# Kernel tuning notes

Hardware: AMD Instinct MI355X
Metric: run time of the kernel (lower is better)

Reference implementation:

```python
import jax, jax.numpy as jnp
import numpy as np

D_MODEL = 2048
HEADS = 16
D_K = D_MODEL // HEADS  # 128
BATCH = 4
SEQ = 2048


def setup_inputs() -> dict:
    key = jax.random.key(0)
    ks = jax.random.split(key, 5)
    scale = (2.0 / (D_MODEL + D_MODEL)) ** 0.5  # trunc-normal std from init
    return {
        "x": jax.random.normal(ks[0], (BATCH, SEQ, D_MODEL), dtype=jnp.float32),
        "W_Q": jax.random.normal(ks[1], (D_MODEL, D_MODEL), dtype=jnp.float32) * scale,
        "W_K": jax.random.normal(ks[2], (D_MODEL, D_MODEL), dtype=jnp.float32) * scale,
        "W_V": jax.random.normal(ks[3], (D_MODEL, D_MODEL), dtype=jnp.float32) * scale,
        "W_O": jax.random.normal(ks[4], (D_MODEL, D_MODEL), dtype=jnp.float32) * scale,
    }


def reference(x, W_Q, W_K, W_V, W_O):
    b, s, d = x.shape
    # weights stored as [(h d_k), d_model] -> [h, d_k, d_model]
    wq = W_Q.reshape(HEADS, D_K, d)
    wk = W_K.reshape(HEADS, D_K, d)
    wv = W_V.reshape(HEADS, D_K, d)
    # projections: [b, h, s, d_k]
    Q = jnp.einsum("hkd,bsd->bhsk", wq, x)
    K = jnp.einsum("hkd,bsd->bhsk", wk, x)
    V = jnp.einsum("hvd,bsd->bhsv", wv, x)
    # causal scaled dot-product attention
    scores = jnp.einsum("bhqk,bhsk->bhqs", Q, K) / jnp.sqrt(jnp.asarray(D_K, x.dtype))
    causal = jnp.tril(jnp.ones((s, s), dtype=bool))  # True -> attend
    scores = jnp.where(causal, scores, jnp.asarray(-jnp.inf, x.dtype))
    attn = jax.nn.softmax(scores, axis=-1)
    mh = jnp.einsum("bhqs,bhsv->bhqv", attn, V)  # [b, h, s, d_v]
    # concat heads -> [b, s, h*d_v]
    mh = jnp.transpose(mh, (0, 2, 1, 3)).reshape(b, s, HEADS * D_K)
    # output projection: W_O is [d_model, (h d_v)]
    out = jnp.einsum("dm,bsm->bsd", W_O, mh)
    return out
```

## Files before the change

### kernel.cpp

```cpp
#include <hip/hip_runtime.h>
#include <stdint.h>

#define D_MODEL 2048
#define HEADS   16
#define DKH     128
#define BATCH   4
#define SEQ     2048
#define MROWS   (BATCH*SEQ)

typedef unsigned short u16;
typedef __attribute__((ext_vector_type(8))) short   short8;
typedef __attribute__((ext_vector_type(4))) float   floatx4;

#define Q_PRESCALE 0.12751744509914576f

__device__ __forceinline__ u16 f2bf(float f) {
  unsigned u = __float_as_uint(f);
  u += 0x7fffu + ((u >> 16) & 1u);
  return (u16)(u >> 16);
}
__device__ __forceinline__ u16 f2bf_fast(float f) {
  return (u16)((__float_as_uint(f) + 0x8000u) >> 16);
}

__device__ __forceinline__ void async_lds16(const u16* g, u16* l) {
  __builtin_amdgcn_global_load_lds(
      (const __attribute__((address_space(1))) unsigned int*)g,
      (__attribute__((address_space(3))) unsigned int*)l, 16, 0, 0);
}

__global__ void cast_all(const float4* __restrict__ x,  const float4* __restrict__ wq,
                         const float4* __restrict__ wk, const float4* __restrict__ wv,
                         const float4* __restrict__ wo, ushort4* __restrict__ dst) {
  int i = blockIdx.x * blockDim.x + threadIdx.x;
  int stride = gridDim.x * blockDim.x;
  for (; i < 8388608; i += stride) {
    const float4* s; int j;
    if (i < 4194304) { s = x; j = i; }
    else {
      int t = i - 4194304; int w = t >> 20; j = t & 1048575;
      s = (w == 0) ? wq : (w == 1) ? wk : (w == 2) ? wv : wo;
    }
    float4 f = s[j];
    ushort4 o;
    o.x = f2bf(f.x); o.y = f2bf(f.y); o.z = f2bf(f.z); o.w = f2bf(f.w);
    dst[i] = o;
  }
}

#define KDIM 2048
#define NKT  32

#define STAGE_A(t, buf) do { \
    const size_t go = (size_t)(t) * 64; \
    const int bo = (buf) * 32768; \
    async_lds16(sA0 + go,          dL0 + bo); \
    async_lds16(sA1 + go,          dL1 + bo); \
    async_lds16(sA0 + go + 262144, dL0 + bo + 8192); \
    async_lds16(sA1 + go + 262144, dL1 + bo + 8192); \
  } while (0)
#define STAGE_B(t, buf) do { \
    const size_t go = (size_t)(t) * 64; \
    const int bo = (buf) * 32768; \
    async_lds16(sB0 + go,          dL0 + bo + 16384); \
    async_lds16(sB1 + go,          dL1 + bo + 16384); \
    async_lds16(sB0 + go + 262144, dL0 + bo + 24576); \
    async_lds16(sB1 + go + 262144, dL1 + bo + 24576); \
  } while (0)

__device__ __forceinline__ void gemm256_core(
    const u16* __restrict__ A, const u16* __restrict__ B,
    u16* __restrict__ S, int rowBase, int colBase, floatx4 acc[8][4])
{
  const int tid  = threadIdx.x;
  const int lane = tid & 63;
  const int w    = tid >> 6;
  const int wm   = w >> 2, wn = w & 3;
  const int c    = lane & 15, quad = lane >> 4;

  const u16 *sA0, *sA1, *sB0, *sB1;
  {
    int L0 = tid * 16, L1 = 8192 + tid * 16;
    int Ls0 = L0 ^ (((L0 >> 7) & 7) << 4);
    int Ls1 = L1 ^ (((L1 >> 7) & 7) << 4);
    sA0 = A + (size_t)(rowBase + (Ls0 >> 7)) * KDIM + ((Ls0 & 127) >> 1);
    sA1 = A + (size_t)(rowBase + (Ls1 >> 7)) * KDIM + ((Ls1 & 127) >> 1);
    sB0 = B + (size_t)(colBase + (Ls0 >> 7)) * KDIM + ((Ls0 & 127) >> 1);
    sB1 = B + (size_t)(colBase + (Ls1 >> 7)) * KDIM + ((Ls1 & 127) >> 1);
  }
  u16* dL0 = S + tid * 8;
  u16* dL1 = S + 4096 + tid * 8;

  const int fo0 = (c * 128 + ((       quad * 16) ^ ((c & 7) << 4))) >> 1;
  const int fo1 = (c * 128 + ((64 +   quad * 16) ^ ((c & 7) << 4))) >> 1;
  const u16* aW = S + wm * 8192;
  const u16* bW = S + 16384 + (wn >> 1) * 8192 + (wn & 1) * 4096;

  const floatx4 z4 = {0.f, 0.f, 0.f, 0.f};
#pragma unroll
  for (int i = 0; i < 8; i++)
#pragma unroll
    for (int j = 0; j < 4; j++) acc[i][j] = z4;

  STAGE_A(0, 0); STAGE_B(0, 0);
  STAGE_A(1, 1); STAGE_B(1, 1);
  asm volatile("s_waitcnt vmcnt(8)" ::: "memory");
  __builtin_amdgcn_s_barrier();

  short8 af[4][2], bf01[2][2], bf23[2][2];

  for (int t = 0; t < NKT; ++t) {
    const int b = t & 1;
    const u16* aB = aW + b * 32768;
    const u16* bB = bW + b * 32768;

#pragma unroll
    for (int i = 0; i < 4; i++) {
      af[i][0] = *(const short8*)(aB + i * 1024 + fo0);
      af[i][1] = *(const short8*)(aB + i * 1024 + fo1);
    }
#pragma unroll
    for (int j = 0; j < 2; j++) {
      bf01[j][0] = *(const short8*)(bB + j * 1024 + fo0);
      bf01[j][1] = *(const short8*)(bB + j * 1024 + fo1);
    }
    if (t >= 1 && t + 1 < NKT) STAGE_B(t + 1, b ^ 1);
    __builtin_amdgcn_s_barrier();
    asm volatile("s_waitcnt lgkmcnt(0)" ::: "memory");
    __builtin_amdgcn_sched_barrier(0);
    __builtin_amdgcn_s_setprio(1);
#pragma unroll
    for (int i = 0; i < 4; i++)
#pragma unroll
      for (int j = 0; j < 2; j++) {
        acc[i][j] = __builtin_amdgcn_mfma_f32_16x16x32_bf16(af[i][0], bf01[j][0], acc[i][j], 0, 0, 0);
        acc[i][j] = __builtin_amdgcn_mfma_f32_16x16x32_bf16(af[i][1], bf01[j][1], acc[i][j], 0, 0, 0);
      }
    __builtin_amdgcn_s_setprio(0);
    __builtin_amdgcn_s_barrier();

#pragma unroll
    for (int j = 0; j < 2; j++) {
      bf23[j][0] = *(const short8*)(bB + (2 + j) * 1024 + fo0);
      bf23[j][1] = *(const short8*)(bB + (2 + j) * 1024 + fo1);
    }
    __builtin_amdgcn_s_barrier();
    asm volatile("s_waitcnt lgkmcnt(0)" ::: "memory");
    __builtin_amdgcn_sched_barrier(0);
    __builtin_amdgcn_s_setprio(1);
#pragma unroll
    for (int i = 0; i < 4; i++)
#pragma unroll
      for (int j = 0; j < 2; j++) {
        acc[i][2 + j] = __builtin_amdgcn_mfma_f32_16x16x32_bf16(af[i][0], bf23[j][0], acc[i][2 + j], 0, 0, 0);
        acc[i][2 + j] = __builtin_amdgcn_mfma_f32_16x16x32_bf16(af[i][1], bf23[j][1], acc[i][2 + j], 0, 0, 0);
      }
    __builtin_amdgcn_s_setprio(0);
    __builtin_amdgcn_s_barrier();

#pragma unroll
    for (int i = 0; i < 4; i++) {
      af[i][0] = *(const short8*)(aB + (4 + i) * 1024 + fo0);
      af[i][1] = *(const short8*)(aB + (4 + i) * 1024 + fo1);
    }
    __builtin_amdgcn_s_barrier();
    asm volatile("s_waitcnt lgkmcnt(0)" ::: "memory");
    __builtin_amdgcn_sched_barrier(0);
    __builtin_amdgcn_s_setprio(1);
#pragma unroll
    for (int i = 0; i < 4; i++)
#pragma unroll
      for (int j = 0; j < 2; j++) {
        acc[4 + i][2 + j] = __builtin_amdgcn_mfma_f32_16x16x32_bf16(af[i][0], bf23[j][0], acc[4 + i][2 + j], 0, 0, 0);
        acc[4 + i][2 + j] = __builtin_amdgcn_mfma_f32_16x16x32_bf16(af[i][1], bf23[j][1], acc[4 + i][2 + j], 0, 0, 0);
      }
    __builtin_amdgcn_s_setprio(0);
    __builtin_amdgcn_s_barrier();

    if (t + 2 < NKT) STAGE_A(t + 2, b);
    __builtin_amdgcn_s_barrier();
    __builtin_amdgcn_s_setprio(1);
#pragma unroll
    for (int i = 0; i < 4; i++)
#pragma unroll
      for (int j = 0; j < 2; j++) {
        acc[4 + i][j] = __builtin_amdgcn_mfma_f32_16x16x32_bf16(af[i][0], bf01[j][0], acc[4 + i][j], 0, 0, 0);
        acc[4 + i][j] = __builtin_amdgcn_mfma_f32_16x16x32_bf16(af[i][1], bf01[j][1], acc[4 + i][j], 0, 0, 0);
      }
    __builtin_amdgcn_s_setprio(0);
    asm volatile("s_waitcnt vmcnt(4)" ::: "memory");
    __builtin_amdgcn_s_barrier();
  }
}

__global__ __launch_bounds__(512, 2) void gemm_qkv(
    const u16* __restrict__ A, const u16* __restrict__ B,
    u16* __restrict__ Qb, u16* __restrict__ Kb, u16* __restrict__ Vpb)
{
  __shared__ __align__(16) u16 S[65536];

  const int tid  = threadIdx.x;
  const int lane = tid & 63;
  const int w    = tid >> 6;
  const int wm   = w >> 2, wn = w & 3;
  const int c    = lane & 15, quad = lane >> 4;
  const int rowBase = blockIdx.x * 256;
  const int colBase = blockIdx.y * 256;

  floatx4 acc[8][4];
  gemm256_core(A, B, S, rowBase, colBase, acc);

  const int proj = colBase >> 11;
  const float esc = (proj == 0) ? Q_PRESCALE : 1.0f;
  u16* dst = (proj == 0) ? Qb : (proj == 1) ? Kb : Vpb;

#pragma unroll
  for (int i = 0; i < 8; i++) {
#pragma unroll
    for (int j = 0; j < 4; j++) {
#pragma unroll
      for (int r = 0; r < 4; r++) {
        int row = rowBase + wm * 128 + i * 16 + quad * 4 + r;
        int col = (colBase & 2047) + wn * 64 + j * 16 + c;
        float v = acc[i][j][r] * esc;
        if (proj < 2) {
          size_t idx = ((size_t)((row >> 11) * HEADS + (col >> 7)) * SEQ + (row & 2047)) * DKH + (col & 127);
          dst[idx] = f2bf(v);
        } else {
          int srow = row & 2047;
          int sp = (srow & ~127) | (((srow & 15) << 3) | ((srow >> 4) & 7));
          size_t idx = ((size_t)((row >> 11) * HEADS + (col >> 7)) * DKH + (col & 127)) * SEQ + sp;
          dst[idx] = f2bf(v);
        }
      }
    }
  }
}

__global__ __launch_bounds__(512, 2) void gemm_out(
    const u16* __restrict__ A, const u16* __restrict__ B,
    float* __restrict__ Cout)
{
  __shared__ __align__(16) u16 S[65536];

  const int tid  = threadIdx.x;
  const int lane = tid & 63;
  const int w    = tid >> 6;
  const int wm   = w >> 2, wn = w & 3;
  const int c    = lane & 15, quad = lane >> 4;
  const int rowBase = blockIdx.x * 256;
  const int colBase = blockIdx.y * 256;

  floatx4 acc[8][4];
  gemm256_core(A, B, S, rowBase, colBase, acc);

#pragma unroll
  for (int i = 0; i < 8; i++)
#pragma unroll
    for (int j = 0; j < 4; j++)
#pragma unroll
      for (int r = 0; r < 4; r++) {
        int row = rowBase + wm * 128 + i * 16 + quad * 4 + r;
        int col = colBase + wn * 64 + j * 16 + c;
        Cout[(size_t)row * D_MODEL + col] = acc[i][j][r];
      }
}

__global__ __launch_bounds__(256, 1) void attn_fwd(
    const u16* __restrict__ Qg, const u16* __restrict__ Kg,
    const u16* __restrict__ Vpg, u16* __restrict__ mh)
{
  __shared__ __align__(16) u16 Sh[2 * 16384 + 16384 + 4 * 32 * 136];

  const int tid  = threadIdx.x;
  const int lane = tid & 63;
  const int w    = tid >> 6;
  const int c    = lane & 15, quad = lane >> 4;
  const int bh   = blockIdx.x;
  const int qt   = 15 - blockIdx.y;
  const int q0   = qt * 128;

  const u16* Qbh = Qg  + (size_t)bh * SEQ * DKH;
  const u16* Kbh = Kg  + (size_t)bh * SEQ * DKH;
  const u16* Vbh = Vpg + (size_t)bh * DKH * SEQ;

  u16* Vs = Sh + 32768;
  u16* Pw = Sh + 49152 + w * 32 * 136;

  const int rowb = tid >> 4;
  const int cbh  = (((tid & 15) ^ (rowb & 7)) << 3);
  const u16* sK = Kbh + rowb * DKH + cbh;
  const u16* sV = Vbh + (size_t)rowb * SEQ + cbh;

  int fof[4];
#pragma unroll
  for (int ks = 0; ks < 4; ks++)
    fof[ks] = ((ks * 64 + quad * 16) ^ ((c & 7) << 4)) >> 1;

#define STAGE_K_ATTN(kbN, buf) do { \
    u16* d_ = Sh + (buf) * 16384 + tid * 8; \
    const u16* s_ = sK + (size_t)(kbN) * DKH; \
    _Pragma("unroll") \
    for (int q_ = 0; q_ < 8; q_++) async_lds16(s_ + q_ * 2048, d_ + q_ * 2048); \
  } while (0)
#define STAGE_V_ATTN(kb_) do { \
    u16* d_ = Vs + tid * 8; \
    const u16* s_ = sV + (kb_); \
    _Pragma("unroll") \
    for (int q_ = 0; q_ < 8; q_++) async_lds16(s_ + (size_t)q_ * 16 * SEQ, d_ + q_ * 2048); \
  } while (0)

  short8 qf[2][4];
#pragma unroll
  for (int m2 = 0; m2 < 2; m2++)
#pragma unroll
    for (int ks = 0; ks < 4; ks++)
      qf[m2][ks] = *(const short8*)&Qbh[(size_t)(q0 + w * 32 + m2 * 16 + c) * DKH + ks * 32 + quad * 8];

  const floatx4 z4 = {0.f, 0.f, 0.f, 0.f};
  floatx4 oacc[2][8];
#pragma unroll
  for (int m2 = 0; m2 < 2; m2++)
#pragma unroll
    for (int d = 0; d < 8; d++) oacc[m2][d] = z4;
  float lrow[2][4];
#pragma unroll
  for (int m2 = 0; m2 < 2; m2++)
#pragma unroll
    for (int r = 0; r < 4; r++) lrow[m2][r] = 0.f;

  STAGE_K_ATTN(0, 0);
  __syncthreads();

  for (int kt = 0; kt <= qt; kt++) {
    const int kb = kt * 128;
    const u16* Kc = Sh + (kt & 1) * 16384;

    STAGE_V_ATTN(kb);
    if (kt < qt) STAGE_K_ATTN(kb + 128, (kt + 1) & 1);

    short8 kf[4][8];
#pragma unroll
    for (int ks = 0; ks < 4; ks++)
#pragma unroll
      for (int n = 0; n < 8; n++)
        kf[ks][n] = *(const short8*)&Kc[(n * 16 + c) * 128 + fof[ks]];

    floatx4 s[2][8];
#pragma unroll
    for (int m2 = 0; m2 < 2; m2++)
#pragma unroll
      for (int n = 0; n < 8; n++) s[m2][n] = z4;
#pragma unroll
    for (int ks = 0; ks < 4; ks++)
#pragma unroll
      for (int n = 0; n < 8; n++) {
        s[0][n] = __builtin_amdgcn_mfma_f32_16x16x32_bf16(qf[0][ks], kf[ks][n], s[0][n], 0, 0, 0);
        s[1][n] = __builtin_amdgcn_mfma_f32_16x16x32_bf16(qf[1][ks], kf[ks][n], s[1][n], 0, 0, 0);
      }

    if (kt == qt) {
#pragma unroll
      for (int m2 = 0; m2 < 2; m2++)
#pragma unroll
        for (int n = 0; n < 8; n++)
#pragma unroll
          for (int r = 0; r < 4; r++) {
            int qrow = w * 32 + m2 * 16 + quad * 4 + r;
            int key  = n * 16 + c;
            if (key > qrow) s[m2][n][r] = -3.0e38f;
          }
    }

#pragma unroll
    for (int m2 = 0; m2 < 2; m2++) {
#pragma unroll
      for (int r = 0; r < 4; r++) {
        float rs = 0.f;
#pragma unroll
        for (int n = 0; n < 8; n++) {
          float p = __builtin_amdgcn_exp2f(s[m2][n][r]);
          s[m2][n][r] = p;
          rs += p;
        }
        rs += __shfl_xor(rs, 1);
        rs += __shfl_xor(rs, 2);
        rs += __shfl_xor(rs, 4);
        rs += __shfl_xor(rs, 8);
        lrow[m2][r] += rs;
      }
    }

#pragma unroll
    for (int m2 = 0; m2 < 2; m2++) {
#pragma unroll
      for (int r = 0; r < 4; r++) {
        short8 pk;
#pragma unroll
        for (int n = 0; n < 8; n++) pk[n] = (short)f2bf_fast(s[m2][n][r]);
        *(short8*)&Pw[(m2 * 16 + quad * 4 + r) * 136 + c * 8] = pk;
      }
    }
    short8 pf[2][4];
#pragma unroll
    for (int m2 = 0; m2 < 2; m2++)
#pragma unroll
      for (int ks = 0; ks < 4; ks++)
        pf[m2][ks] = *(const short8*)&Pw[(m2 * 16 + c) * 136 + ks * 32 + quad * 8];

    __syncthreads();

    short8 vf[8][4];
#pragma unroll
    for (int d = 0; d < 8; d++)
#pragma unroll
      for (int ks = 0; ks < 4; ks++)
        vf[d][ks] = *(const short8*)&Vs[(d * 16 + c) * 128 + fof[ks]];

#pragma unroll
    for (int d = 0; d < 8; d++)
#pragma unroll
      for (int ks = 0; ks < 4; ks++) {
        oacc[0][d] = __builtin_amdgcn_mfma_f32_16x16x32_bf16(pf[0][ks], vf[d][ks], oacc[0][d], 0, 0, 0);
        oacc[1][d] = __builtin_amdgcn_mfma_f32_16x16x32_bf16(pf[1][ks], vf[d][ks], oacc[1][d], 0, 0, 0);
      }

    __syncthreads();
  }

  const int b = bh >> 4, h = bh & 15;
#pragma unroll
  for (int m2 = 0; m2 < 2; m2++) {
#pragma unroll
    for (int r = 0; r < 4; r++) {
      float rl = 1.0f / lrow[m2][r];
      int qrow = q0 + w * 32 + m2 * 16 + quad * 4 + r;
      u16* dst = mh + ((size_t)(b * SEQ + qrow)) * D_MODEL + h * DKH;
#pragma unroll
      for (int d = 0; d < 8; d++)
        dst[d * 16 + c] = f2bf(oacc[m2][d][r] * rl);
    }
  }
}

extern "C" void kernel_launch(void* const* d_in, const int* in_sizes, int n_in,
                              void* d_out, int out_size, void* d_ws, size_t ws_size,
                              hipStream_t stream) {
  const float* x  = (const float*)d_in[0];
  const float* wq = (const float*)d_in[1];
  const float* wk = (const float*)d_in[2];
  const float* wv = (const float*)d_in[3];
  const float* wo = (const float*)d_in[4];
  float* out = (float*)d_out;

  u16* ws  = (u16*)d_ws;
  u16* xb  = ws;
  u16* wqb = xb  + 16777216;
  u16* wkb = wqb + 4194304;
  u16* wvb = wkb + 4194304;
  u16* wob = wvb + 4194304;
  u16* Qb  = wob + 4194304;
  u16* Kb  = Qb  + 16777216;
  u16* Vpb = Kb  + 16777216;
  u16* mhb = Vpb + 16777216;

  cast_all<<<4096, 256, 0, stream>>>((const float4*)x,  (const float4*)wq,
                                     (const float4*)wk, (const float4*)wv,
                                     (const float4*)wo, (ushort4*)xb);

  gemm_qkv<<<dim3(32, 24), 512, 0, stream>>>(xb, wqb, Qb, Kb, Vpb);

  attn_fwd<<<dim3(64, 16), 256, 0, stream>>>(Qb, Kb, Vpb, mhb);

  gemm_out<<<dim3(32, 8), 512, 0, stream>>>(mhb, wob, out);
}
```

Before: 599.0 us.

## Restructure GEMM main loop into two phases with register-prefetched A fragments

Replaces the four-quadrant MFMA schedule, which had many barriers and partial LDS reads, with two halves. All B fragments and the second half of A are loaded up front, and the next tile's first A half is prefetched into registers while the second-half MFMAs run. A and B staging for t+2 is now issued together after a full vmcnt(0)/lgkmcnt(0) wait. This cuts barrier count and aims to overlap LDS reads with MFMA. In exchange it raises register pressure and adds a full global-load drain each iteration, which could expose memory latency.

```diff
diff --git a/kernel.cpp b/kernel.cpp
--- a/kernel.cpp
+++ b/kernel.cpp
@@ -107,7 +107,13 @@
   asm volatile("s_waitcnt vmcnt(8)" ::: "memory");
   __builtin_amdgcn_s_barrier();
 
-  short8 af[4][2], bf01[2][2], bf23[2][2];
+  short8 aX[4][2], aY[4][2], bf[4][2];
+
+#pragma unroll
+  for (int i = 0; i < 4; i++) {
+    aX[i][0] = *(const short8*)(aW + i * 1024 + fo0);
+    aX[i][1] = *(const short8*)(aW + i * 1024 + fo1);
+  }
 
   for (int t = 0; t < NKT; ++t) {
     const int b = t & 1;
@@ -115,81 +121,52 @@
     const u16* bB = bW + b * 32768;
 
 #pragma unroll
+    for (int j = 0; j < 4; j++) {
+      bf[j][0] = *(const short8*)(bB + j * 1024 + fo0);
+      bf[j][1] = *(const short8*)(bB + j * 1024 + fo1);
+    }
+#pragma unroll
     for (int i = 0; i < 4; i++) {
-      af[i][0] = *(const short8*)(aB + i * 1024 + fo0);
-      af[i][1] = *(const short8*)(aB + i * 1024 + fo1);
-    }
-#pragma unroll
-    for (int j = 0; j < 2; j++) {
-      bf01[j][0] = *(const short8*)(bB + j * 1024 + fo0);
-      bf01[j][1] = *(const short8*)(bB + j * 1024 + fo1);
-    }
-    if (t >= 1 && t + 1 < NKT) STAGE_B(t + 1, b ^ 1);
-    __builtin_amdgcn_s_barrier();
-    asm volatile("s_waitcnt lgkmcnt(0)" ::: "memory");
+      aY[i][0] = *(const short8*)(aB + (4 + i) * 1024 + fo0);
+      aY[i][1] = *(const short8*)(aB + (4 + i) * 1024 + fo1);
+    }
+
+    asm volatile("s_waitcnt lgkmcnt(8)" ::: "memory");
     __builtin_amdgcn_sched_barrier(0);
     __builtin_amdgcn_s_setprio(1);
 #pragma unroll
     for (int i = 0; i < 4; i++)
 #pragma unroll
-      for (int j = 0; j < 2; j++) {
-        acc[i][j] = __builtin_amdgcn_mfma_f32_16x16x32_bf16(af[i][0], bf01[j][0], acc[i][j], 0, 0, 0);
-        acc[i][j] = __builtin_amdgcn_mfma_f32_16x16x32_bf16(af[i][1], bf01[j][1], acc[i][j], 0, 0, 0);
+      for (int j = 0; j < 4; j++) {
+        acc[i][j] = __builtin_amdgcn_mfma_f32_16x16x32_bf16(aX[i][0], bf[j][0], acc[i][j], 0, 0, 0);
+        acc[i][j] = __builtin_amdgcn_mfma_f32_16x16x32_bf16(aX[i][1], bf[j][1], acc[i][j], 0, 0, 0);
       }
     __builtin_amdgcn_s_setprio(0);
+
+    asm volatile("s_waitcnt lgkmcnt(0)" ::: "memory");
+    asm volatile("s_waitcnt vmcnt(0)" ::: "memory");
     __builtin_amdgcn_s_barrier();
 
-#pragma unroll
-    for (int j = 0; j < 2; j++) {
-      bf23[j][0] = *(const short8*)(bB + (2 + j) * 1024 + fo0);
-      bf23[j][1] = *(const short8*)(bB + (2 + j) * 1024 + fo1);
-    }
-    __builtin_amdgcn_s_barrier();
-    asm volatile("s_waitcnt lgkmcnt(0)" ::: "memory");
+    if (t + 2 < NKT) { STAGE_A(t + 2, b); STAGE_B(t + 2, b); }
+
+    if (t + 1 < NKT) {
+      const u16* aN = aW + (b ^ 1) * 32768;
+#pragma unroll
+      for (int i = 0; i < 4; i++) {
+        aX[i][0] = *(const short8*)(aN + i * 1024 + fo0);
+        aX[i][1] = *(const short8*)(aN + i * 1024 + fo1);
+      }
+    }
     __builtin_amdgcn_sched_barrier(0);
     __builtin_amdgcn_s_setprio(1);
 #pragma unroll
     for (int i = 0; i < 4; i++)
 #pragma unroll
-      for (int j = 0; j < 2; j++) {
-        acc[i][2 + j] = __builtin_amdgcn_mfma_f32_16x16x32_bf16(af[i][0], bf23[j][0], acc[i][2 + j], 0, 0, 0);
-        acc[i][2 + j] = __builtin_amdgcn_mfma_f32_16x16x32_bf16(af[i][1], bf23[j][1], acc[i][2 + j], 0, 0, 0);
+      for (int j = 0; j < 4; j++) {
+        acc[4 + i][j] = __builtin_amdgcn_mfma_f32_16x16x32_bf16(aY[i][0], bf[j][0], acc[4 + i][j], 0, 0, 0);
+        acc[4 + i][j] = __builtin_amdgcn_mfma_f32_16x16x32_bf16(aY[i][1], bf[j][1], acc[4 + i][j], 0, 0, 0);
       }
     __builtin_amdgcn_s_setprio(0);
-    __builtin_amdgcn_s_barrier();
-
-#pragma unroll
-    for (int i = 0; i < 4; i++) {
-      af[i][0] = *(const short8*)(aB + (4 + i) * 1024 + fo0);
-      af[i][1] = *(const short8*)(aB + (4 + i) * 1024 + fo1);
-    }
-    __builtin_amdgcn_s_barrier();
-    asm volatile("s_waitcnt lgkmcnt(0)" ::: "memory");
-    __builtin_amdgcn_sched_barrier(0);
-    __builtin_amdgcn_s_setprio(1);
-#pragma unroll
-    for (int i = 0; i < 4; i++)
-#pragma unroll
-      for (int j = 0; j < 2; j++) {
-        acc[4 + i][2 + j] = __builtin_amdgcn_mfma_f32_16x16x32_bf16(af[i][0], bf23[j][0], acc[4 + i][2 + j], 0, 0, 0);
-        acc[4 + i][2 + j] = __builtin_amdgcn_mfma_f32_16x16x32_bf16(af[i][1], bf23[j][1], acc[4 + i][2 + j], 0, 0, 0);
-      }
-    __builtin_amdgcn_s_setprio(0);
-    __builtin_amdgcn_s_barrier();
-
-    if (t + 2 < NKT) STAGE_A(t + 2, b);
-    __builtin_amdgcn_s_barrier();
-    __builtin_amdgcn_s_setprio(1);
-#pragma unroll
-    for (int i = 0; i < 4; i++)
-#pragma unroll
-      for (int j = 0; j < 2; j++) {
-        acc[4 + i][j] = __builtin_amdgcn_mfma_f32_16x16x32_bf16(af[i][0], bf01[j][0], acc[4 + i][j], 0, 0, 0);
-        acc[4 + i][j] = __builtin_amdgcn_mfma_f32_16x16x32_bf16(af[i][1], bf01[j][1], acc[4 + i][j], 0, 0, 0);
-      }
-    __builtin_amdgcn_s_setprio(0);
-    asm volatile("s_waitcnt vmcnt(4)" ::: "memory");
-    __builtin_amdgcn_s_barrier();
   }
 }
 
```

Measured after the change: 586.7 us. -2.1%, faster.
